# Performance work log

Measured on AMD Instinct MI355X. Metric: run time of the kernel, lower is better.

## Reference

```python
import jax, jax.numpy as jnp
import numpy as np

D_EMBED, D_K, D_V = 1024, 64, 64
B, S = 4, 4096


def setup_inputs() -> dict:
    key = jax.random.key(0)
    k1, k2, k3, k4 = jax.random.split(key, 4)
    x = jax.random.normal(k1, (B, S, D_EMBED), dtype=jnp.float32)
    # nn.Linear(d_embed, d) stores weight as [d, d_embed]
    Wq = jax.random.normal(k2, (D_K, D_EMBED), dtype=jnp.float32) * (D_EMBED ** -0.5)
    Wk = jax.random.normal(k3, (D_K, D_EMBED), dtype=jnp.float32) * (D_EMBED ** -0.5)
    Wv = jax.random.normal(k4, (D_V, D_EMBED), dtype=jnp.float32) * (D_EMBED ** -0.5)
    return {"x": x, "Wq": Wq, "Wk": Wk, "Wv": Wv}


def reference(x, Wq, Wk, Wv):
    # self-attention: y = z = x
    key = jnp.einsum('bse,ke->bsk', x, Wk)
    query = jnp.einsum('bse,ke->bsk', x, Wq)
    value = jnp.einsum('bse,ve->bsv', x, Wv)
    d_k = key.shape[-1]
    weight = jnp.einsum('bqk,bsk->bqs', query, key) / (d_k ** 0.5)
    # Faithful to torch: tril then masked_fill(weight == 0, -inf)
    weight = jnp.tril(weight)
    weight = jnp.where(weight == 0, -jnp.inf, weight)
    weight = jax.nn.softmax(weight, axis=-1)
    return jnp.einsum('bqs,bsv->bqv', weight, value)
```

## Files before the change

kernel.cpp:

```cpp
#include <hip/hip_runtime.h>
#include <hip/hip_bf16.h>


typedef short s16x8 __attribute__((ext_vector_type(8)));
typedef float f32x4 __attribute__((ext_vector_type(4)));
typedef float f32x16 __attribute__((ext_vector_type(16)));
typedef unsigned u32x2 __attribute__((ext_vector_type(2)));
typedef union { unsigned u[4]; s16x8 v; } pfrag;

#define MFMA16(a, b, c) __builtin_amdgcn_mfma_f32_16x16x32_bf16(a, b, c, 0, 0, 0)
#define MFMA32(a, b, c) __builtin_amdgcn_mfma_f32_32x32x16_bf16(a, b, c, 0, 0, 0)

constexpr int SEQ = 4096;
constexpr int DE  = 1024;

__device__ __forceinline__ short f2bf(float f) {
    union { float f; unsigned u; } v; v.f = f;
    unsigned r = (v.u + 0x7FFFu + ((v.u >> 16) & 1u)) >> 16;
    return (short)r;
}
__device__ __forceinline__ unsigned fbits(float f) { union { float f; unsigned u; } v; v.f = f; return v.u; }
__device__ __forceinline__ float bitsf(unsigned u) { union { unsigned u; float f; } v; v.u = u; return v.f; }
__device__ __forceinline__ unsigned pk2(float a, float b) {
    return (fbits(b) & 0xFFFF0000u) | (fbits(a) >> 16);
}

#define GLDS(gp, lp)                                                          \
    __builtin_amdgcn_global_load_lds(                                         \
        (const __attribute__((address_space(1))) unsigned int*)(gp),          \
        (__attribute__((address_space(3))) unsigned int*)(lp), 16, 0, 0)

__global__ __launch_bounds__(256) void k_convw(const float* __restrict__ Wq,
                                               const float* __restrict__ Wk,
                                               const float* __restrict__ Wv,
                                               short* __restrict__ Wb) {
    int i = (blockIdx.x * 256 + threadIdx.x) * 4;
    if (i >= 192 * 1024) return;
    int n = i >> 10, k = i & 1023;
    const float* src; float sc;
    if (n < 64)       { src = Wq + n * 1024;         sc = 0.18033688011112042f; }
    else if (n < 128) { src = Wk + (n - 64) * 1024;  sc = 1.0f; }
    else              { src = Wv + (n - 128) * 1024; sc = 1.0f; }
    float4 v = *(const float4*)(src + k);
    short4 o;
    o.x = f2bf(v.x * sc); o.y = f2bf(v.y * sc);
    o.z = f2bf(v.z * sc); o.w = f2bf(v.w * sc);
    *(short4*)(Wb + i) = o;
}

__global__ __launch_bounds__(512) void k_proj(const float* __restrict__ x,
                                              const short* __restrict__ Wb,
                                              short* __restrict__ Qs,
                                              short* __restrict__ Ks,
                                              short* __restrict__ Vt) {
    __shared__ __align__(16) char lds[2][40960];
    const int tid  = threadIdx.x;
    const int lane = tid & 63;
    const int c = lane & 15, g = (lane >> 4) & 3;
    const int wv = tid >> 6;
    const int rg = wv & 3, nh = wv >> 2;
    const int n0 = nh * 96;
    const int m0 = blockIdx.x * 64;

    const int Ar  = tid >> 4;
    const int Acs = ((tid & 15) << 4) ^ ((Ar & 7) << 4);
    const char* aS0 = (const char*)x + (((size_t)(m0 + Ar)) << 12) + Acs;
    const char* aS1 = aS0 + ((size_t)32 << 12);
    const int Wr  = tid >> 3;
    const int Wcs = ((tid & 7) << 4) ^ ((Wr & 7) << 4);
    const char* wS0 = (const char*)Wb + (((size_t)Wr) << 11) + Wcs;
    const char* wS1 = wS0 + ((size_t)64 << 11);
    const char* wS2 = wS0 + ((size_t)128 << 11);

    char* db0 = &lds[0][0] + tid * 16;
    char* db1 = &lds[1][0] + tid * 16;

    const int arow = rg * 16 + c;
    const int swz  = (c & 7) << 4;
    const char* aR[2] = { &lds[0][0] + arow * 256, &lds[1][0] + arow * 256 };
    const char* wR[2][6];
#pragma unroll
    for (int nf = 0; nf < 6; nf++) {
        int wrow = n0 + nf * 16 + c;
        wR[0][nf] = &lds[0][0] + 16384 + wrow * 128;
        wR[1][nf] = &lds[1][0] + 16384 + wrow * 128;
    }

    f32x4 acc[6];
#pragma unroll
    for (int i = 0; i < 6; i++) acc[i] = (f32x4){0.f, 0.f, 0.f, 0.f};

#define PSTAGE(kk, db) {                                  \
        GLDS(aS0 + (kk) * 256, (db));                     \
        GLDS(aS1 + (kk) * 256, (db) + 8192);              \
        GLDS(wS0 + (kk) * 128, (db) + 16384);             \
        GLDS(wS1 + (kk) * 128, (db) + 24576);             \
        GLDS(wS2 + (kk) * 128, (db) + 32768); }

#define PCOMPUTE(bi) {                                                         \
        _Pragma("unroll")                                                      \
        for (int kc = 0; kc < 2; kc++) {                                       \
            float4 a0 = *(const float4*)(aR[bi] + ((kc*128 + g*32)      ^ swz)); \
            float4 a1 = *(const float4*)(aR[bi] + ((kc*128 + g*32 + 16) ^ swz)); \
            s16x8 a;                                                           \
            a[0]=f2bf(a0.x); a[1]=f2bf(a0.y); a[2]=f2bf(a0.z); a[3]=f2bf(a0.w); \
            a[4]=f2bf(a1.x); a[5]=f2bf(a1.y); a[6]=f2bf(a1.z); a[7]=f2bf(a1.w); \
            _Pragma("unroll")                                                  \
            for (int nf = 0; nf < 6; nf++) {                                   \
                s16x8 bfr = *(const s16x8*)(wR[bi][nf] + ((kc*64 + g*16) ^ swz)); \
                acc[nf] = MFMA16(a, bfr, acc[nf]);                             \
            }                                                                  \
        } }

    PSTAGE(0, db0);
    PSTAGE(1, db1);

    for (int kk = 0; kk < 15; kk++) {
        asm volatile("s_waitcnt vmcnt(5)" ::: "memory");
        __builtin_amdgcn_sched_barrier(0);
        __builtin_amdgcn_s_barrier();
        if (kk & 1) PCOMPUTE(1) else PCOMPUTE(0)
        asm volatile("s_waitcnt lgkmcnt(0)" ::: "memory");
        __builtin_amdgcn_sched_barrier(0);
        __builtin_amdgcn_s_barrier();
        if (kk < 14) { if (kk & 1) PSTAGE(kk + 2, db1) else PSTAGE(kk + 2, db0) }
    }
    asm volatile("s_waitcnt vmcnt(0)" ::: "memory");
    __builtin_amdgcn_sched_barrier(0);
    __builtin_amdgcn_s_barrier();
    PCOMPUTE(1)
#undef PSTAGE
#undef PCOMPUTE

#pragma unroll
    for (int nf = 0; nf < 6; nf++) {
        int col16 = n0 + nf * 16;
        if (col16 < 64) {
            int col = col16 + c;
#pragma unroll
            for (int r = 0; r < 4; r++)
                Qs[(size_t)(m0 + rg * 16 + g * 4 + r) * 64 + col] = f2bf(acc[nf][r]);
        } else if (col16 < 128) {
            int col = col16 - 64 + c;
#pragma unroll
            for (int r = 0; r < 4; r++)
                Ks[(size_t)(m0 + rg * 16 + g * 4 + r) * 64 + col] = f2bf(acc[nf][r]);
        } else {
            int d  = col16 - 128 + c;
            int mm = m0 + rg * 16 + g * 4;
            int bt = mm >> 12, s0 = mm & (SEQ - 1);
            short4 o;
            o.x = f2bf(acc[nf][0]); o.y = f2bf(acc[nf][1]);
            o.z = f2bf(acc[nf][2]); o.w = f2bf(acc[nf][3]);
            *(short4*)(Vt + ((size_t)(bt * 64 + d)) * SEQ + s0) = o;
        }
    }
}

#define SMTREE(sa, sb, m, ll, o0, o1) {                                        \
    float mx8[8];                                                              \
    _Pragma("unroll")                                                          \
    for (int i2 = 0; i2 < 8; i2++)                                             \
        mx8[i2] = fmaxf(fmaxf(sa[i2], sa[i2 + 8]), fmaxf(sb[i2], sb[i2 + 8])); \
    float tm_ = fmaxf(fmaxf(fmaxf(mx8[0], mx8[1]), fmaxf(mx8[2], mx8[3])),     \
                      fmaxf(fmaxf(mx8[4], mx8[5]), fmaxf(mx8[6], mx8[7])));    \
    u32x2 sw_ = __builtin_amdgcn_permlane32_swap(fbits(tm_), fbits(tm_), false, false); \
    tm_ = fmaxf(bitsf(sw_[0]), bitsf(sw_[1]));                                 \
    float mn_ = fmaxf(m, tm_);                                                 \
    float sc_ = __builtin_amdgcn_exp2f(m - mn_);                               \
    m = mn_;                                                                   \
    _Pragma("unroll")                                                          \
    for (int i2 = 0; i2 < 16; i2++) {                                          \
        sa[i2] = __builtin_amdgcn_exp2f(sa[i2] - mn_);                         \
        sb[i2] = __builtin_amdgcn_exp2f(sb[i2] - mn_);                         \
    }                                                                          \
    float s8_[8];                                                              \
    _Pragma("unroll")                                                          \
    for (int i2 = 0; i2 < 8; i2++)                                             \
        s8_[i2] = (sa[i2] + sa[i2 + 8]) + (sb[i2] + sb[i2 + 8]);               \
    float ss_ = ((s8_[0] + s8_[1]) + (s8_[2] + s8_[3]))                        \
              + ((s8_[4] + s8_[5]) + (s8_[6] + s8_[7]));                       \
    sw_ = __builtin_amdgcn_permlane32_swap(fbits(ss_), fbits(ss_), false, false); \
    ss_ = bitsf(sw_[0]) + bitsf(sw_[1]);                                       \
    ll = ll * sc_ + ss_;                                                       \
    o0 *= sc_; o1 *= sc_; }

#define PACKPH(sa, sb, u0, u1, u2, u3) {                                       \
    unsigned A0 = pk2(sa[0], sa[1]),   B0 = pk2(sa[2], sa[3]);                 \
    unsigned A1 = pk2(sa[4], sa[5]),   B1 = pk2(sa[6], sa[7]);                 \
    unsigned A2 = pk2(sa[8], sa[9]),   B2 = pk2(sa[10], sa[11]);               \
    unsigned A3 = pk2(sa[12], sa[13]), B3 = pk2(sa[14], sa[15]);               \
    u32x2 r0_ = __builtin_amdgcn_permlane32_swap(A0, A1, false, false);        \
    u32x2 r1_ = __builtin_amdgcn_permlane32_swap(B0, B1, false, false);        \
    u32x2 r2_ = __builtin_amdgcn_permlane32_swap(A2, A3, false, false);        \
    u32x2 r3_ = __builtin_amdgcn_permlane32_swap(B2, B3, false, false);        \
    u0.u[0] = r0_[0]; u0.u[1] = r1_[0]; u0.u[2] = r0_[1]; u0.u[3] = r1_[1];    \
    u1.u[0] = r2_[0]; u1.u[1] = r3_[0]; u1.u[2] = r2_[1]; u1.u[3] = r3_[1];    \
    A0 = pk2(sb[0], sb[1]);   B0 = pk2(sb[2], sb[3]);                          \
    A1 = pk2(sb[4], sb[5]);   B1 = pk2(sb[6], sb[7]);                          \
    A2 = pk2(sb[8], sb[9]);   B2 = pk2(sb[10], sb[11]);                        \
    A3 = pk2(sb[12], sb[13]); B3 = pk2(sb[14], sb[15]);                        \
    r0_ = __builtin_amdgcn_permlane32_swap(A0, A1, false, false);              \
    r1_ = __builtin_amdgcn_permlane32_swap(B0, B1, false, false);              \
    r2_ = __builtin_amdgcn_permlane32_swap(A2, A3, false, false);              \
    r3_ = __builtin_amdgcn_permlane32_swap(B2, B3, false, false);              \
    u2.u[0] = r0_[0]; u2.u[1] = r1_[0]; u2.u[2] = r0_[1]; u2.u[3] = r1_[1];    \
    u3.u[0] = r2_[0]; u3.u[1] = r3_[0]; u3.u[2] = r2_[1]; u3.u[3] = r3_[1]; }

__global__ __launch_bounds__(256, 2) void k_attn(const short* __restrict__ Qs,
                                                 const short* __restrict__ Ks,
                                                 const short* __restrict__ Vt,
                                                 float* __restrict__ pws) {
    __shared__ __align__(16) char smem[2][16384];

    int tid = threadIdx.x;
    int l = tid & 63, wv = tid >> 6;
    int q = l & 31, hi = l >> 5;

    int ub = blockIdx.x >> 2, bt = blockIdx.x & 3;
    int u = ub, j = 31, cs = 8;
    while (u >= cs) { u -= cs; --j; cs = (j + 4) >> 2; }
    int seg = u;
    int kb0 = seg << 9;
    int kend_t = min(j * 128 + 128, kb0 + 512);
    const int R = (kend_t - kb0 + 63) >> 6;
    const int q0 = j * 128 + wv * 32;
    const int mycend = q0 + 32;

    const short* Qb = Qs + (size_t)bt * SEQ * 64;
    const short* Kb = Ks + (size_t)bt * SEQ * 64;
    const short* Vb = Vt + (size_t)bt * 64 * SEQ;

    s16x8 qf[4];
#pragma unroll
    for (int d = 0; d < 4; d++)
        qf[d] = *(const s16x8*)(Qb + (size_t)(q0 + q) * 64 + d * 16 + hi * 8);

    const int row8 = l >> 3;
    const int scs  = (l & 7) ^ row8;

#define ASTAGE(kb, b) {                                                        \
        _Pragma("unroll")                                                      \
        for (int i = 0; i < 2; i++) {                                          \
            GLDS(Kb + (((size_t)((kb) + wv*16 + i*8 + row8)) << 6) + scs*8,    \
                 &smem[b][0] + (wv*16 + i*8)*128);                             \
            GLDS(Vb + (size_t)(wv*16 + i*8 + row8) * SEQ + (kb) + scs*8,       \
                 &smem[b][0] + 8192 + (wv*16 + i*8)*128); } }

    f32x16 o0 = {}, o1 = {};
    float m = -1e30f, ll = 0.f;
    const int qs7 = q & 7;

    ASTAGE(kb0, 0);
    if (R > 1) ASTAGE(kb0 + 64, 1);

    for (int r = 0; r < R; r++) {
        if (r == R - 1) asm volatile("s_waitcnt vmcnt(0)" ::: "memory");
        else            asm volatile("s_waitcnt vmcnt(4)" ::: "memory");
        __builtin_amdgcn_sched_barrier(0);
        __builtin_amdgcn_s_barrier();

        const char* kl = &smem[r & 1][0];
        const char* vl = kl + 8192;
        s16x8 kf[8], vf[8];
#pragma unroll
        for (int dd = 0; dd < 4; dd++) {
            int ch = ((2 * dd + hi) ^ qs7) << 4;
            kf[dd]     = *(const s16x8*)(kl + q * 128 + ch);
            kf[4 + dd] = *(const s16x8*)(kl + (32 + q) * 128 + ch);
            vf[dd]     = *(const s16x8*)(vl + q * 128 + ch);
            vf[4 + dd] = *(const s16x8*)(vl + (32 + q) * 128 + ch);
        }
        asm volatile("s_waitcnt lgkmcnt(0)" ::: "memory");
        __builtin_amdgcn_sched_barrier(0);
        __builtin_amdgcn_s_barrier();
        if (r + 2 < R) { if (r & 1) ASTAGE(kb0 + (r + 2) * 64, 1) else ASTAGE(kb0 + (r + 2) * 64, 0) }

        int k0 = kb0 + r * 64;
        if (k0 < mycend) {
            f32x16 sa = {}, sb = {};
            __builtin_amdgcn_s_setprio(1);
#pragma unroll
            for (int dd = 0; dd < 4; dd++) {
                sa = MFMA32(kf[dd],     qf[dd], sa);
                sb = MFMA32(kf[4 + dd], qf[dd], sb);
            }
            __builtin_amdgcn_s_setprio(0);
            if (k0 + 31 > q0) {
#pragma unroll
                for (int rr = 0; rr < 16; rr++) {
                    int kv = k0 + (rr & 3) + 8 * (rr >> 2) + 4 * hi;
                    if (kv > q0 + q) sa[rr] = -3.0e38f;
                }
            }
            if (k0 + 63 > q0) {
#pragma unroll
                for (int rr = 0; rr < 16; rr++) {
                    int kv = k0 + 32 + (rr & 3) + 8 * (rr >> 2) + 4 * hi;
                    if (kv > q0 + q) sb[rr] = -3.0e38f;
                }
            }
            SMTREE(sa, sb, m, ll, o0, o1);
            pfrag u0_, u1_, u2_, u3_;
            PACKPH(sa, sb, u0_, u1_, u2_, u3_);
            __builtin_amdgcn_s_setprio(1);
            o0 = MFMA32(vf[0], u0_.v, o0);
            o0 = MFMA32(vf[1], u1_.v, o0);
            o0 = MFMA32(vf[2], u2_.v, o0);
            o0 = MFMA32(vf[3], u3_.v, o0);
            o1 = MFMA32(vf[4], u0_.v, o1);
            o1 = MFMA32(vf[5], u1_.v, o1);
            o1 = MFMA32(vf[6], u2_.v, o1);
            o1 = MFMA32(vf[7], u3_.v, o1);
            __builtin_amdgcn_s_setprio(0);
        }
    }
#undef ASTAGE

    float* p = pws + ((((size_t)(bt * 32 + j) * 4 + wv) * 8 + seg)) * 2112;
#pragma unroll
    for (int rr = 0; rr < 16; rr++) {
        int dv = (rr & 3) + 8 * (rr >> 2) + 4 * hi;
        p[dv * 32 + q]        = o0[rr];
        p[(dv + 32) * 32 + q] = o1[rr];
    }
    if (hi == 0) { p[2048 + q] = m; p[2080 + q] = ll; }
}

__global__ __launch_bounds__(256) void k_comb(const float* __restrict__ pws,
                                              float* __restrict__ out) {
    int b = blockIdx.x;
    int w = b & 3, j = (b >> 2) & 31, bt = b >> 7;
    int nseg = (j + 4) >> 2;

    int tid = threadIdx.x;
    int q = tid >> 3, dv0 = (tid & 7) * 8;
    const float* base = pws + ((size_t)(bt * 32 + j) * 4 + w) * 8 * 2112;

    float ms[8], wsg[8];
    float M = -1e30f;
#pragma unroll
    for (int s = 0; s < 8; s++) {
        if (s < nseg) { ms[s] = base[s * 2112 + 2048 + q]; M = fmaxf(M, ms[s]); }
    }
    float L = 0.f;
#pragma unroll
    for (int s = 0; s < 8; s++) {
        if (s < nseg) {
            wsg[s] = __builtin_amdgcn_exp2f(ms[s] - M);
            L += wsg[s] * base[s * 2112 + 2080 + q];
        }
    }
    float inv = 1.0f / L;
    float res[8];
#pragma unroll
    for (int i = 0; i < 8; i++) res[i] = 0.f;
#pragma unroll
    for (int s = 0; s < 8; s++) {
        if (s < nseg) {
            const float* po = base + s * 2112;
#pragma unroll
            for (int i = 0; i < 8; i++) res[i] += wsg[s] * po[(dv0 + i) * 32 + q];
        }
    }
    float* op = out + ((size_t)bt * SEQ + j * 128 + w * 32 + q) * 64 + dv0;
    float4 f0 = {res[0] * inv, res[1] * inv, res[2] * inv, res[3] * inv};
    float4 f1 = {res[4] * inv, res[5] * inv, res[6] * inv, res[7] * inv};
    *(float4*)op = f0;
    *(float4*)(op + 4) = f1;
}

extern "C" void kernel_launch(void* const* d_in, const int* in_sizes, int n_in,
                              void* d_out, int out_size, void* d_ws, size_t ws_size,
                              hipStream_t stream) {
    const float* x  = (const float*)d_in[0];
    const float* Wq = (const float*)d_in[1];
    const float* Wk = (const float*)d_in[2];
    const float* Wv = (const float*)d_in[3];
    float* out = (float*)d_out;

    char* ws = (char*)d_ws;
    short* Wb = (short*)ws;
    short* Qs = (short*)(ws + 393216);
    short* Ks = (short*)(ws + 393216 + 2097152);
    short* Vt = (short*)(ws + 393216 + 2 * 2097152);
    float* pP = (float*)(ws + 6684672);

    k_convw<<<dim3(192), dim3(256), 0, stream>>>(Wq, Wk, Wv, Wb);
    k_proj <<<dim3(256), dim3(512), 0, stream>>>(x, Wb, Qs, Ks, Vt);
    k_attn <<<dim3(576), dim3(256), 0, stream>>>(Qs, Ks, Vt, pP);
    k_comb <<<dim3(512), dim3(256), 0, stream>>>(pP, out);
}
```

Before: 68.43 us.

## Stage K/V via registers into LDS and use lazy softmax rescaling

Replaces the direct global-to-LDS async loads with a register-staged pipeline: the next tile is loaded into registers two iterations ahead and written into the swizzled LDS buffer at the top of each iteration, leaving one barrier per iteration instead of two. Also switches the online softmax to a lazy rescale that only updates the running max and rescales accumulators when any lane's max grows by more than a threshold, skipping rescale work on most tiles. This costs extra VGPRs for the staging registers and a wave-wide vote. With the lazy threshold the unnormalised exponentials can reach up to 2^8 before packing to bf16.

```diff
diff --git a/kernel.cpp b/kernel.cpp
--- a/kernel.cpp
+++ b/kernel.cpp
@@ -156,34 +156,6 @@
         }
     }
 }
-
-#define SMTREE(sa, sb, m, ll, o0, o1) {                                        \
-    float mx8[8];                                                              \
-    _Pragma("unroll")                                                          \
-    for (int i2 = 0; i2 < 8; i2++)                                             \
-        mx8[i2] = fmaxf(fmaxf(sa[i2], sa[i2 + 8]), fmaxf(sb[i2], sb[i2 + 8])); \
-    float tm_ = fmaxf(fmaxf(fmaxf(mx8[0], mx8[1]), fmaxf(mx8[2], mx8[3])),     \
-                      fmaxf(fmaxf(mx8[4], mx8[5]), fmaxf(mx8[6], mx8[7])));    \
-    u32x2 sw_ = __builtin_amdgcn_permlane32_swap(fbits(tm_), fbits(tm_), false, false); \
-    tm_ = fmaxf(bitsf(sw_[0]), bitsf(sw_[1]));                                 \
-    float mn_ = fmaxf(m, tm_);                                                 \
-    float sc_ = __builtin_amdgcn_exp2f(m - mn_);                               \
-    m = mn_;                                                                   \
-    _Pragma("unroll")                                                          \
-    for (int i2 = 0; i2 < 16; i2++) {                                          \
-        sa[i2] = __builtin_amdgcn_exp2f(sa[i2] - mn_);                         \
-        sb[i2] = __builtin_amdgcn_exp2f(sb[i2] - mn_);                         \
-    }                                                                          \
-    float s8_[8];                                                              \
-    _Pragma("unroll")                                                          \
-    for (int i2 = 0; i2 < 8; i2++)                                             \
-        s8_[i2] = (sa[i2] + sa[i2 + 8]) + (sb[i2] + sb[i2 + 8]);               \
-    float ss_ = ((s8_[0] + s8_[1]) + (s8_[2] + s8_[3]))                        \
-              + ((s8_[4] + s8_[5]) + (s8_[6] + s8_[7]));                       \
-    sw_ = __builtin_amdgcn_permlane32_swap(fbits(ss_), fbits(ss_), false, false); \
-    ss_ = bitsf(sw_[0]) + bitsf(sw_[1]);                                       \
-    ll = ll * sc_ + ss_;                                                       \
-    o0 *= sc_; o1 *= sc_; }
 
 #define PACKPH(sa, sb, u0, u1, u2, u3) {                                       \
     unsigned A0 = pk2(sa[0], sa[1]),   B0 = pk2(sa[2], sa[3]);                 \
@@ -236,29 +208,37 @@
     for (int d = 0; d < 4; d++)
         qf[d] = *(const s16x8*)(Qb + (size_t)(q0 + q) * 64 + d * 16 + hi * 8);
 
-    const int row8 = l >> 3;
-    const int scs  = (l & 7) ^ row8;
-
-#define ASTAGE(kb, b) {                                                        \
-        _Pragma("unroll")                                                      \
-        for (int i = 0; i < 2; i++) {                                          \
-            GLDS(Kb + (((size_t)((kb) + wv*16 + i*8 + row8)) << 6) + scs*8,    \
-                 &smem[b][0] + (wv*16 + i*8)*128);                             \
-            GLDS(Vb + (size_t)(wv*16 + i*8 + row8) * SEQ + (kb) + scs*8,       \
-                 &smem[b][0] + 8192 + (wv*16 + i*8)*128); } }
+    const int g0r = (tid * 2) >> 3,     g0c = (tid * 2) & 7;
+    const int g1r = (tid * 2 + 1) >> 3, g1c = (tid * 2 + 1) & 7;
+    const int kofs0 = g0r * 128 + ((g0c ^ (g0r & 7)) << 4);
+    const int kofs1 = g1r * 128 + ((g1c ^ (g1r & 7)) << 4);
+
+    s16x8 kreg0, kreg1, vreg0, vreg1;
+#define LOADREGS(kb) {                                                         \
+        kreg0 = *(const s16x8*)(Kb + (size_t)((kb) + g0r) * 64 + g0c * 8);     \
+        kreg1 = *(const s16x8*)(Kb + (size_t)((kb) + g1r) * 64 + g1c * 8);     \
+        vreg0 = *(const s16x8*)(Vb + (size_t)g0r * SEQ + (kb) + g0c * 8);      \
+        vreg1 = *(const s16x8*)(Vb + (size_t)g1r * SEQ + (kb) + g1c * 8); }
+#define WRITELDS(b) {                                                          \
+        *(s16x8*)(&smem[b][0] + kofs0) = kreg0;                                \
+        *(s16x8*)(&smem[b][0] + kofs1) = kreg1;                                \
+        *(s16x8*)(&smem[b][0] + 8192 + kofs0) = vreg0;                         \
+        *(s16x8*)(&smem[b][0] + 8192 + kofs1) = vreg1; }
 
     f32x16 o0 = {}, o1 = {};
     float m = -1e30f, ll = 0.f;
     const int qs7 = q & 7;
 
-    ASTAGE(kb0, 0);
-    if (R > 1) ASTAGE(kb0 + 64, 1);
+    LOADREGS(kb0);
+    WRITELDS(0);
+    if (R > 1) LOADREGS(kb0 + 64);
+    asm volatile("s_waitcnt lgkmcnt(0)" ::: "memory");
+    __builtin_amdgcn_sched_barrier(0);
+    __builtin_amdgcn_s_barrier();
 
     for (int r = 0; r < R; r++) {
-        if (r == R - 1) asm volatile("s_waitcnt vmcnt(0)" ::: "memory");
-        else            asm volatile("s_waitcnt vmcnt(4)" ::: "memory");
-        __builtin_amdgcn_sched_barrier(0);
-        __builtin_amdgcn_s_barrier();
+        if (r + 1 < R) WRITELDS((r + 1) & 1);
+        if (r + 2 < R) LOADREGS(kb0 + (r + 2) * 64);
 
         const char* kl = &smem[r & 1][0];
         const char* vl = kl + 8192;
@@ -273,8 +253,6 @@
         }
         asm volatile("s_waitcnt lgkmcnt(0)" ::: "memory");
         __builtin_amdgcn_sched_barrier(0);
-        __builtin_amdgcn_s_barrier();
-        if (r + 2 < R) { if (r & 1) ASTAGE(kb0 + (r + 2) * 64, 1) else ASTAGE(kb0 + (r + 2) * 64, 0) }
 
         int k0 = kb0 + r * 64;
         if (k0 < mycend) {
@@ -300,7 +278,30 @@
                     if (kv > q0 + q) sb[rr] = -3.0e38f;
                 }
             }
-            SMTREE(sa, sb, m, ll, o0, o1);
+            float t0 = -3.0e38f, t1 = -3.0e38f;
+#pragma unroll
+            for (int rr = 0; rr < 16; rr++) { t0 = fmaxf(t0, sa[rr]); t1 = fmaxf(t1, sb[rr]); }
+            float tm = fmaxf(t0, t1);
+            u32x2 sw = __builtin_amdgcn_permlane32_swap(fbits(tm), fbits(tm), false, false);
+            tm = fmaxf(bitsf(sw[0]), bitsf(sw[1]));
+            if (__any(tm > m + 8.0f)) {
+                float mn = fmaxf(m, tm);
+                float sc_ = __builtin_amdgcn_exp2f(m - mn);
+                m = mn;
+                ll *= sc_;
+                o0 *= sc_; o1 *= sc_;
+            }
+            float ss = 0.f;
+#pragma unroll
+            for (int rr = 0; rr < 16; rr++) {
+                sa[rr] = __builtin_amdgcn_exp2f(sa[rr] - m);
+                sb[rr] = __builtin_amdgcn_exp2f(sb[rr] - m);
+                ss += sa[rr] + sb[rr];
+            }
+            sw = __builtin_amdgcn_permlane32_swap(fbits(ss), fbits(ss), false, false);
+            ss = bitsf(sw[0]) + bitsf(sw[1]);
+            ll += ss;
+
             pfrag u0_, u1_, u2_, u3_;
             PACKPH(sa, sb, u0_, u1_, u2_, u3_);
             __builtin_amdgcn_s_setprio(1);
@@ -314,8 +315,11 @@
             o1 = MFMA32(vf[7], u3_.v, o1);
             __builtin_amdgcn_s_setprio(0);
         }
-    }
-#undef ASTAGE
+
+        __builtin_amdgcn_s_barrier();
+    }
+#undef LOADREGS
+#undef WRITELDS
 
     float* p = pws + ((((size_t)(bt * 32 + j) * 4 + wv) * 8 + seg)) * 2112;
 #pragma unroll
```

New measurement: 72.23 us. 1.06x slower.
